# Optimization experiments

Measured on AMD Instinct MI355X. Metric: run time of the kernel, lower is better.

Reference implementation:

```python
import jax, jax.numpy as jnp
import numpy as np

N_FFT = 8192  # config.n (next power of two of 2*seq_len)


def setup_inputs() -> dict:
    key = jax.random.key(0)
    k1, k2, k3, k4 = jax.random.split(key, 4)
    x = jax.random.normal(k1, (2, 4096, 128), dtype=jnp.float32)
    spectral_filters = jax.random.normal(k2, (4096, 16), dtype=jnp.float32)
    # nn.Parameter tensors (zeros in torch init; randomized for a meaningful test)
    M_phi_plus = jax.random.normal(k3, (16, 128, 128), dtype=jnp.float32) * 0.02
    M_phi_minus = jax.random.normal(k4, (16, 128, 128), dtype=jnp.float32) * 0.02
    return {
        "x": x,
        "spectral_filters": spectral_filters,
        "M_phi_plus": M_phi_plus,
        "M_phi_minus": M_phi_minus,
    }


def reference(x, spectral_filters, M_phi_plus, M_phi_minus):
    # STU forward, use_tensordot=False, use_hankel_L=False.
    B, L, D = x.shape
    K = spectral_filters.shape[1]
    n = N_FFT

    # sgn[l] = (-1)^l : the "negative featurization" sign flip
    sgn = jnp.where(jnp.arange(L) % 2 == 0, 1.0, -1.0).astype(x.dtype)  # (L,)

    # FFT of the K spectral filters: (F, K), F = n//2 + 1
    Vf = jnp.fft.rfft(spectral_filters, n=n, axis=0)

    # FFTs of u and sign-flipped u (convolution is linear, so we avoid the
    # torch expand to (B, L, K, D) before the FFT): (B, F, D)
    Uf_plus = jnp.fft.rfft(x, n=n, axis=1)
    Uf_minus = jnp.fft.rfft(x * sgn[None, :, None], n=n, axis=1)

    # Pointwise multiply in frequency, broadcast over K and D: (B, F, K, D)
    U_plus = jnp.fft.irfft(Vf[None, :, :, None] * Uf_plus[:, :, None, :], n=n, axis=1)[:, :L]
    U_minus = jnp.fft.irfft(Vf[None, :, :, None] * Uf_minus[:, :, None, :], n=n, axis=1)[:, :L]
    U_minus = U_minus * sgn[None, :, None, None]  # undo sign on outputs

    # Contract (B, L, K, D) with (K, D, D_out)  ==  reshape(B,L,K*D) @ (K*D, D_out)
    spectral_plus = jnp.einsum("blkd,kde->ble", U_plus, M_phi_plus)
    spectral_minus = jnp.einsum("blkd,kde->ble", U_minus, M_phi_minus)
    return spectral_plus + spectral_minus
```

## Files before the change

### kernel.cpp

```cpp
#include <hip/hip_runtime.h>
#include <stdint.h>

#define N2   8192
#define N    4096
#define LOGN 12
#define F_TOT 4097
#define FP    4112
#define D    128
#define K    16
#define B    2
#define PI_F 3.14159265358979323846f

typedef _Float16 f16x8 __attribute__((ext_vector_type(8)));
typedef float    f32x4 __attribute__((ext_vector_type(4)));

__device__ __forceinline__ void gload_lds16(const void* g, void* l) {
  __builtin_amdgcn_global_load_lds((const __attribute__((address_space(1))) uint32_t*)g,
                                   (__attribute__((address_space(3))) uint32_t*)l, 16, 0, 0);
}

__device__ __forceinline__ int swz(int w) { return w ^ ((w >> 6) & 31); }

__device__ __forceinline__ _Float16 hpick(uint32_t w, int hi) {
  union { unsigned short u; _Float16 h; } c;
  c.u = (unsigned short)(hi ? (w >> 16) : (w & 0xffffu));
  return c.h;
}

__device__ __forceinline__ uint32_t packh2(float a, float b) {
  union { uint32_t u; unsigned short s[2]; } p;
  union { unsigned short u; _Float16 h; } ca, cb;
  ca.h = (_Float16)a; cb.h = (_Float16)b;
  p.s[0] = ca.u; p.s[1] = cb.u;
  return p.u;
}

__device__ __forceinline__ void fft_lds(float* re, float* im, const float2* tw,
                                        int tid, int nthr, float sign) {
  for (int s = 0; s < LOGN; ++s) {
    int len = 1 << s;
    for (int t = tid; t < (N >> 1); t += nthr) {
      int j = t & (len - 1);
      int base = ((t >> s) << (s + 1)) + j;
      int i0 = swz(base), i1 = swz(base + len);
      float2 w = tw[len + j];
      float wr = w.x, wi = sign * w.y;
      float ar = re[i0], ai = im[i0];
      float br = re[i1], bi = im[i1];
      float tr = wr * br - wi * bi;
      float ti = wr * bi + wi * br;
      re[i0] = ar + tr;  im[i0] = ai + ti;
      re[i1] = ar - tr;  im[i1] = ai - ti;
    }
    __syncthreads();
  }
}

__device__ __forceinline__ void fill_tw(float2* tw, int tid, int nthr) {
  for (int i = tid; i < N; i += nthr) {
    if (i >= 1) {
      int s = 31 - __clz(i);
      int j = i - (1 << s);
      float ang = PI_F * (float)j / (float)(1 << s);
      float wi_, wr_; __sincosf(ang, &wi_, &wr_);
      tw[i] = make_float2(wr_, wi_);
    }
  }
}

__global__ __launch_bounds__(256) void transpose_x(const float* __restrict__ x,
                                                   float* __restrict__ xT) {
  __shared__ float t[32][33];
  const int b = blockIdx.z;
  const int l0 = blockIdx.x * 32, d0 = blockIdx.y * 32;
  const int c = threadIdx.x & 31, r0 = threadIdx.x >> 5;
#pragma unroll
  for (int i = 0; i < 4; ++i) {
    int r = r0 + i * 8;
    t[r][c] = x[((size_t)b * N + l0 + r) * D + d0 + c];
  }
  __syncthreads();
#pragma unroll
  for (int i = 0; i < 4; ++i) {
    int r = r0 + i * 8;
    xT[((size_t)b * D + d0 + r) * N + l0 + c] = t[c][r];
  }
}

__global__ __launch_bounds__(512) void fwd_fft(const float* __restrict__ xT,
                                               const float* __restrict__ filt,
                                               const float* __restrict__ Mp,
                                               const float* __restrict__ Mm,
                                               uint32_t* __restrict__ Ufh,
                                               float2* __restrict__ Vf,
                                               _Float16* __restrict__ Mt) {
  __shared__ float re[N];
  __shared__ float im[N];
  __shared__ float2 tw[N];
  const int tid = threadIdx.x;
  const int sig = blockIdx.x;

  if (sig >= B * D + K) {
    const int pid = sig - (B * D + K);
    const int k = pid & 15, h = pid >> 4;
    const float* src = (h ? Mm : Mp) + (size_t)k * D * D;
    for (int d0 = 0; d0 < D; d0 += 16) {
      for (int i = tid; i < 16 * D; i += 512) re[i] = src[(size_t)d0 * D + i];
      __syncthreads();
      if (tid < 256) {
        const int e = tid >> 1, c0 = (tid & 1) * 8;
        f16x8 w;
#pragma unroll
        for (int j = 0; j < 8; ++j) w[j] = (_Float16)re[(c0 + j) * D + e];
        const int eq = e >> 5, el = e & 31;
        const size_t kd8 = (size_t)(d0 + c0) >> 3;
        *(f16x8*)(Mt + (((((size_t)h * 4 + eq) * K + k) * 16 + kd8) * 32 + el) * 8) = w;
      }
      __syncthreads();
    }
    return;
  }

  fill_tw(tw, tid, 512);

  const float* in; int istride;
  int b = 0, d = 0, k = 0;
  const bool isx = sig < B * D;
  if (isx) { b = sig >> 7; d = sig & (D - 1); in = xT + ((size_t)b * D + d) * N; istride = 1; }
  else     { k = sig - B * D; in = filt + k; istride = K; }

  for (int m = tid; m < N; m += 512) {
    float vr = 0.f, vi = 0.f;
    if (m < (N >> 1)) {
      if (istride == 1) { float2 z = ((const float2*)in)[m]; vr = z.x; vi = z.y; }
      else { vr = in[(size_t)(2 * m) * istride]; vi = in[(size_t)(2 * m + 1) * istride]; }
    }
    int dst = swz(__brev(m) >> (32 - LOGN));
    re[dst] = vr; im[dst] = vi;
  }
  __syncthreads();
  fft_lds(re, im, tw, tid, 512, -1.0f);

  for (int f = tid; f <= (N >> 1); f += 512) {
    int f2 = f & (N - 1), fn = (N - f) & (N - 1);
    float zr = re[swz(f2)], zi = im[swz(f2)];
    float nr = re[swz(fn)], ni = im[swz(fn)];
    float Er = 0.5f * (zr + nr), Ei = 0.5f * (zi - ni);
    float Or = 0.5f * (zi + ni), Oi = -0.5f * (zr - nr);
    float ang = -PI_F * (float)f / (float)N;
    float wi_, wr_; __sincosf(ang, &wi_, &wr_);
    float X0r = Er + wr_ * Or - wi_ * Oi;
    float X0i = Ei + wr_ * Oi + wi_ * Or;
    float X1r = Er - wr_ * Or + wi_ * Oi;
    float X1i = -Ei + wr_ * Oi + wi_ * Or;
    if (isx) {
      uint32_t* o = Ufh + ((size_t)b * F_TOT) * D + d;
      o[(size_t)f * D]       = packh2(X0r, X0i);
      o[(size_t)(N - f) * D] = packh2(X1r, X1i);
    } else {
      Vf[(size_t)f * K + k]       = make_float2(X0r, X0i);
      Vf[(size_t)(N - f) * K + k] = make_float2(X1r, X1i);
    }
  }
}

__global__ __launch_bounds__(256, 3) void middle_mfma(const uint32_t* __restrict__ Ufh,
                                                      const float2* __restrict__ Vf,
                                                      const _Float16* __restrict__ Mt,
                                                      float2* __restrict__ Gt) {
  __shared__ __align__(16) char smem[24576];
  float2*   Vl   = (float2*)smem;
  char*     bbuf = smem + 8192;

  const int tid = threadIdx.x;
  const int l = tid & 63, w = tid >> 6;
  const int l15 = l & 15, g = l >> 4;
  const int fg = w >> 1, eg = w & 1;
  const int eq = blockIdx.y, ks = blockIdx.z;
  const int fx = blockIdx.x * 32;
  const int fo = l15 >> 2, bb = (l15 >> 1) & 1, ri = l15 & 1;

  auto STAGE = [&](int buf, int st) {
    const int kg = ks * 8 + (st >> 1), pm = st & 1;
    const _Float16* tile = Mt + (((size_t)pm * 4 + eq) * K + kg) * 4096;
#pragma unroll
    for (int i = 0; i < 2; ++i) {
      const int off = w * 1024 + i * 512;
      gload_lds16((const void*)(tile + off + l * 8),
                  (void*)(bbuf + (size_t)buf * 8192 + (size_t)off * 2));
    }
  };
  STAGE(0, 0);

  {
    const int fl = tid >> 3, kq = tid & 7;
    int fe = fx + fl; if (fe > N) fe = N;
    *(float4*)&Vl[((size_t)0 * 32 + fl) * 16 + kq * 2] =
        *(const float4*)&Vf[(size_t)fe * K + kq * 2];
    *(float4*)&Vl[((size_t)1 * 32 + fl) * 16 + kq * 2] =
        *(const float4*)&Vf[(size_t)(N - fe) * K + kq * 2];
  }

  f16x8 A[4][4];
#pragma unroll
  for (int s = 0; s < 4; ++s) {
    int f = fx + fg * 16 + s * 4 + fo; if (f > N) f = N;
    const uint4* ur = (const uint4*)(Ufh + ((size_t)bb * F_TOT + f) * D);
#pragma unroll
    for (int ds = 0; ds < 4; ++ds) {
      uint4 w0 = ur[ds * 8 + g * 2];
      uint4 w1 = ur[ds * 8 + g * 2 + 1];
      f16x8 a;
      a[0] = hpick(w0.x, ri); a[1] = hpick(w0.y, ri);
      a[2] = hpick(w0.z, ri); a[3] = hpick(w0.w, ri);
      a[4] = hpick(w1.x, ri); a[5] = hpick(w1.y, ri);
      a[6] = hpick(w1.z, ri); a[7] = hpick(w1.w, ri);
      A[s][ds] = a;
    }
  }

  f32x4 acc[4];
#pragma unroll
  for (int s = 0; s < 4; ++s) acc[s] = (f32x4)0.f;

  asm volatile("s_waitcnt vmcnt(0)" ::: "memory");
  __syncthreads();

  int buf = 0;
  for (int st = 0; st < 16; ++st) {
    if (st < 15) STAGE(buf ^ 1, st + 1);
    const int kg = ks * 8 + (st >> 1), pm = st & 1;
    const _Float16* bc = (const _Float16*)(bbuf + (size_t)buf * 8192);

    float2 vv[4];
#pragma unroll
    for (int s = 0; s < 4; ++s)
      vv[s] = Vl[((size_t)pm * 32 + fg * 16 + s * 4 + g) * 16 + kg];

    f32x4 P[4];
#pragma unroll
    for (int ds = 0; ds < 4; ++ds) {
      f16x8 bf = *(const f16x8*)(bc + (size_t)((ds * 4 + g) * 32 + eg * 16 + l15) * 8);
#pragma unroll
      for (int s = 0; s < 4; ++s) {
        f32x4 cin = (ds == 0) ? (f32x4)0.f : P[s];
        P[s] = __builtin_amdgcn_mfma_f32_16x16x32_f16(A[s][ds], bf, cin, 0, 0, 0);
      }
    }
#pragma unroll
    for (int s = 0; s < 4; ++s) {
      const float vr = vv[s].x, vy = vv[s].y;
      if (pm == 0) {
        acc[s][0] += vr * P[s][0] - vy * P[s][1];
        acc[s][1] += vy * P[s][0] + vr * P[s][1];
        acc[s][2] += vr * P[s][2] - vy * P[s][3];
        acc[s][3] += vy * P[s][2] + vr * P[s][3];
      } else {
        acc[s][0] += vr * P[s][0] + vy * P[s][1];
        acc[s][1] += vr * P[s][1] - vy * P[s][0];
        acc[s][2] += vr * P[s][2] + vy * P[s][3];
        acc[s][3] += vr * P[s][3] - vy * P[s][2];
      }
    }
    asm volatile("s_waitcnt vmcnt(0)" ::: "memory");
    __syncthreads();
    buf ^= 1;
  }

  float2* tr = (float2*)smem;
#pragma unroll
  for (int s = 0; s < 4; ++s) {
    const int fl = fg * 16 + s * 4 + g;
    const int el = eg * 16 + l15;
    tr[(size_t)el * 33 + fl]        = make_float2(acc[s][0], acc[s][1]);
    tr[(size_t)(32 + el) * 33 + fl] = make_float2(acc[s][2], acc[s][3]);
  }
  __syncthreads();
  const size_t slab = (size_t)ks * B * D * FP;
#pragma unroll
  for (int p = 0; p < 4; ++p) {
    const int row = p * 16 + (tid >> 4);
    const int bo = row >> 5, e_gl = eq * 32 + (row & 31);
    const int c = (tid & 15) * 2;
    const int fgl = fx + c;
    if (fgl < F_TOT) {
      float2 v0 = tr[(size_t)row * 33 + c], v1 = tr[(size_t)row * 33 + c + 1];
      *(float4*)&Gt[slab + ((size_t)bo * D + e_gl) * FP + fgl] =
          make_float4(v0.x, v0.y, v1.x, v1.y);
    }
  }
}

__global__ __launch_bounds__(512) void inv_fft(const float2* __restrict__ Gt,
                                               float* __restrict__ out) {
  __shared__ float re[N];
  __shared__ float im[N];
  __shared__ float2 tw[N];
  const int tid = threadIdx.x;
  const int sig = blockIdx.x;
  const int b = sig >> 7, e = sig & (D - 1);
  const float2* g0 = Gt + ((size_t)b * D + e) * FP;
  const size_t pstr = (size_t)B * D * FP;

  fill_tw(tw, tid, 512);

  for (int kk = tid; kk <= (N >> 1); kk += 512) {
    float2 a0 = g0[kk],     a1 = g0[pstr + kk];
    float2 b0 = g0[N - kk], b1 = g0[pstr + (N - kk)];
    float Xkx = a0.x + a1.x, Xky = a0.y + a1.y;
    float Xnx = b0.x + b1.x, Xny = b0.y + b1.y;
    float Er = 0.5f * (Xkx + Xnx), Ei = 0.5f * (Xky - Xny);
    float Dr = 0.5f * (Xkx - Xnx), Di = 0.5f * (Xky + Xny);
    float ang = PI_F * (float)kk / (float)N;
    float wi_, wr_; __sincosf(ang, &wi_, &wr_);
    float Or = Dr * wr_ - Di * wi_;
    float Oi = Dr * wi_ + Di * wr_;
    int d1 = swz(__brev(kk) >> (32 - LOGN));
    re[d1] = Er - Oi; im[d1] = Ei + Or;
    if (kk != 0 && kk != (N >> 1)) {
      int d2 = swz(__brev(N - kk) >> (32 - LOGN));
      re[d2] = Er + Oi; im[d2] = -Ei + Or;
    }
  }
  __syncthreads();
  fft_lds(re, im, tw, tid, 512, +1.0f);
  const float scale = 1.0f / (float)N;
  float* ob = out + (size_t)b * N * D + e;
  for (int m = tid; m < (N >> 1); m += 512) {
    int i0 = swz(m);
    ob[(size_t)(2 * m) * D]     = re[i0] * scale;
    ob[(size_t)(2 * m + 1) * D] = im[i0] * scale;
  }
}

extern "C" void kernel_launch(void* const* d_in, const int* in_sizes, int n_in,
                              void* d_out, int out_size, void* d_ws, size_t ws_size,
                              hipStream_t stream) {
  const float* x  = (const float*)d_in[0];
  const float* fl = (const float*)d_in[1];
  const float* Mp = (const float*)d_in[2];
  const float* Mm = (const float*)d_in[3];
  float* out = (float*)d_out;

  float*    xT  = (float*)d_ws;
  uint32_t* Ufh = (uint32_t*)(xT + (size_t)B * D * N);
  float2*   Vf  = (float2*)(Ufh + (size_t)B * F_TOT * D);
  float2*   Gt  = Vf + (size_t)F_TOT * K;
  _Float16* Mt  = (_Float16*)(Gt + (size_t)2 * B * D * FP);

  transpose_x<<<dim3(N / 32, D / 32, B), 256, 0, stream>>>(x, xT);
  fwd_fft<<<B * D + K + 32, 512, 0, stream>>>(xT, fl, Mp, Mm, Ufh, Vf, Mt);
  middle_mfma<<<dim3(129, 4, 2), 256, 0, stream>>>(Ufh, Vf, Mt, Gt);
  inv_fft<<<B * D, 512, 0, stream>>>(Gt, out);
}
```

Baseline: 85.70 us.

## Use radix-4 LDS FFT, padded LDS indexing, and transposed output with separate transpose

The in-LDS FFT moves from radix-2 to radix-4 stages, halving the number of passes and __syncthreads barriers. The XOR swizzle is replaced by padding one word per 32 elements to avoid bank conflicts. The inverse FFT now writes contiguous float2 rows into a scratch buffer (reusing xT), and a new transpose kernel produces the (B,L,D) output, replacing the strided scattered stores. This trades one extra kernel launch and a round trip through global memory for coalesced writes and fewer FFT stages.

```diff
diff --git a/kernel.cpp b/kernel.cpp
--- a/kernel.cpp
+++ b/kernel.cpp
@@ -10,6 +10,7 @@
 #define K    16
 #define B    2
 #define PI_F 3.14159265358979323846f
+#define NPAD (N + (N >> 5))
 
 typedef _Float16 f16x8 __attribute__((ext_vector_type(8)));
 typedef float    f32x4 __attribute__((ext_vector_type(4)));
@@ -19,7 +20,7 @@
                                    (__attribute__((address_space(3))) uint32_t*)l, 16, 0, 0);
 }
 
-__device__ __forceinline__ int swz(int w) { return w ^ ((w >> 6) & 31); }
+__device__ __forceinline__ int pad(int w) { return w + (w >> 5); }
 
 __device__ __forceinline__ _Float16 hpick(uint32_t w, int hi) {
   union { unsigned short u; _Float16 h; } c;
@@ -35,36 +36,49 @@
   return p.u;
 }
 
+__device__ __forceinline__ void fill_tw(float2* tw, int tid, int nthr) {
+  for (int i = tid + 1; i < N; i += nthr) {
+    int s = 31 - __clz(i);
+    int j = i - (1 << s);
+    float ang = PI_F * (float)j / (float)(1 << s);
+    float wi_, wr_; __sincosf(ang, &wi_, &wr_);
+    tw[i] = make_float2(wr_, wi_);
+  }
+}
+
 __device__ __forceinline__ void fft_lds(float* re, float* im, const float2* tw,
                                         int tid, int nthr, float sign) {
-  for (int s = 0; s < LOGN; ++s) {
-    int len = 1 << s;
-    for (int t = tid; t < (N >> 1); t += nthr) {
-      int j = t & (len - 1);
-      int base = ((t >> s) << (s + 1)) + j;
-      int i0 = swz(base), i1 = swz(base + len);
-      float2 w = tw[len + j];
-      float wr = w.x, wi = sign * w.y;
-      float ar = re[i0], ai = im[i0];
-      float br = re[i1], bi = im[i1];
-      float tr = wr * br - wi * bi;
-      float ti = wr * bi + wi * br;
-      re[i0] = ar + tr;  im[i0] = ai + ti;
-      re[i1] = ar - tr;  im[i1] = ai - ti;
+  for (int s = 0; s < LOGN; s += 2) {
+    const int len = 1 << s;
+    for (int t = tid; t < (N >> 2); t += nthr) {
+      const int j = t & (len - 1);
+      const int base = ((t >> s) << (s + 2)) + j;
+      const int i0 = pad(base), i1 = pad(base + len);
+      const int i2 = pad(base + 2 * len), i3 = pad(base + 3 * len);
+      float2 w1 = tw[len + j];
+      float2 w2 = tw[2 * len + j];
+      float2 w3 = tw[3 * len + j];
+      const float w1r = w1.x, w1i = sign * w1.y;
+      const float w2r = w2.x, w2i = sign * w2.y;
+      const float w3r = w3.x, w3i = sign * w3.y;
+      float x0r = re[i0], x0i = im[i0];
+      float x1r = re[i1], x1i = im[i1];
+      float x2r = re[i2], x2i = im[i2];
+      float x3r = re[i3], x3i = im[i3];
+      float t1r = w1r * x1r - w1i * x1i, t1i = w1r * x1i + w1i * x1r;
+      float t3r = w1r * x3r - w1i * x3i, t3i = w1r * x3i + w1i * x3r;
+      float b0r = x0r + t1r, b0i = x0i + t1i;
+      float b1r = x0r - t1r, b1i = x0i - t1i;
+      float b2r = x2r + t3r, b2i = x2i + t3i;
+      float b3r = x2r - t3r, b3i = x2i - t3i;
+      float u2r = w2r * b2r - w2i * b2i, u2i = w2r * b2i + w2i * b2r;
+      float u3r = w3r * b3r - w3i * b3i, u3i = w3r * b3i + w3i * b3r;
+      re[i0] = b0r + u2r; im[i0] = b0i + u2i;
+      re[i2] = b0r - u2r; im[i2] = b0i - u2i;
+      re[i1] = b1r + u3r; im[i1] = b1i + u3i;
+      re[i3] = b1r - u3r; im[i3] = b1i - u3i;
     }
     __syncthreads();
-  }
-}
-
-__device__ __forceinline__ void fill_tw(float2* tw, int tid, int nthr) {
-  for (int i = tid; i < N; i += nthr) {
-    if (i >= 1) {
-      int s = 31 - __clz(i);
-      int j = i - (1 << s);
-      float ang = PI_F * (float)j / (float)(1 << s);
-      float wi_, wr_; __sincosf(ang, &wi_, &wr_);
-      tw[i] = make_float2(wr_, wi_);
-    }
   }
 }
 
@@ -84,6 +98,25 @@
   for (int i = 0; i < 4; ++i) {
     int r = r0 + i * 8;
     xT[((size_t)b * D + d0 + r) * N + l0 + c] = t[c][r];
+  }
+}
+
+__global__ __launch_bounds__(256) void transpose_out(const float* __restrict__ outT,
+                                                     float* __restrict__ out) {
+  __shared__ float t[32][33];
+  const int b = blockIdx.z;
+  const int l0 = blockIdx.x * 32, d0 = blockIdx.y * 32;
+  const int c = threadIdx.x & 31, r0 = threadIdx.x >> 5;
+#pragma unroll
+  for (int i = 0; i < 4; ++i) {
+    int r = r0 + i * 8;
+    t[r][c] = outT[((size_t)b * D + d0 + r) * N + l0 + c];
+  }
+  __syncthreads();
+#pragma unroll
+  for (int i = 0; i < 4; ++i) {
+    int r = r0 + i * 8;
+    out[((size_t)b * N + l0 + r) * D + d0 + c] = t[c][r];
   }
 }
 
@@ -94,8 +127,8 @@
                                                uint32_t* __restrict__ Ufh,
                                                float2* __restrict__ Vf,
                                                _Float16* __restrict__ Mt) {
-  __shared__ float re[N];
-  __shared__ float im[N];
+  __shared__ float re[NPAD];
+  __shared__ float im[NPAD];
   __shared__ float2 tw[N];
   const int tid = threadIdx.x;
   const int sig = blockIdx.x;
@@ -135,7 +168,7 @@
       if (istride == 1) { float2 z = ((const float2*)in)[m]; vr = z.x; vi = z.y; }
       else { vr = in[(size_t)(2 * m) * istride]; vi = in[(size_t)(2 * m + 1) * istride]; }
     }
-    int dst = swz(__brev(m) >> (32 - LOGN));
+    int dst = pad(__brev(m) >> (32 - LOGN));
     re[dst] = vr; im[dst] = vi;
   }
   __syncthreads();
@@ -143,8 +176,8 @@
 
   for (int f = tid; f <= (N >> 1); f += 512) {
     int f2 = f & (N - 1), fn = (N - f) & (N - 1);
-    float zr = re[swz(f2)], zi = im[swz(f2)];
-    float nr = re[swz(fn)], ni = im[swz(fn)];
+    float zr = re[pad(f2)], zi = im[pad(f2)];
+    float nr = re[pad(fn)], ni = im[pad(fn)];
     float Er = 0.5f * (zr + nr), Ei = 0.5f * (zi - ni);
     float Or = 0.5f * (zi + ni), Oi = -0.5f * (zr - nr);
     float ang = -PI_F * (float)f / (float)N;
@@ -292,9 +325,9 @@
 }
 
 __global__ __launch_bounds__(512) void inv_fft(const float2* __restrict__ Gt,
-                                               float* __restrict__ out) {
-  __shared__ float re[N];
-  __shared__ float im[N];
+                                               float* __restrict__ outT) {
+  __shared__ float re[NPAD];
+  __shared__ float im[NPAD];
   __shared__ float2 tw[N];
   const int tid = threadIdx.x;
   const int sig = blockIdx.x;
@@ -315,21 +348,20 @@
     float wi_, wr_; __sincosf(ang, &wi_, &wr_);
     float Or = Dr * wr_ - Di * wi_;
     float Oi = Dr * wi_ + Di * wr_;
-    int d1 = swz(__brev(kk) >> (32 - LOGN));
+    int d1 = pad(__brev(kk) >> (32 - LOGN));
     re[d1] = Er - Oi; im[d1] = Ei + Or;
     if (kk != 0 && kk != (N >> 1)) {
-      int d2 = swz(__brev(N - kk) >> (32 - LOGN));
+      int d2 = pad(__brev(N - kk) >> (32 - LOGN));
       re[d2] = Er + Oi; im[d2] = -Ei + Or;
     }
   }
   __syncthreads();
   fft_lds(re, im, tw, tid, 512, +1.0f);
   const float scale = 1.0f / (float)N;
-  float* ob = out + (size_t)b * N * D + e;
+  float2* ob = (float2*)(outT + ((size_t)b * D + e) * N);
   for (int m = tid; m < (N >> 1); m += 512) {
-    int i0 = swz(m);
-    ob[(size_t)(2 * m) * D]     = re[i0] * scale;
-    ob[(size_t)(2 * m + 1) * D] = im[i0] * scale;
+    int i0 = pad(m);
+    ob[m] = make_float2(re[i0] * scale, im[i0] * scale);
   }
 }
 
@@ -351,5 +383,6 @@
   transpose_x<<<dim3(N / 32, D / 32, B), 256, 0, stream>>>(x, xT);
   fwd_fft<<<B * D + K + 32, 512, 0, stream>>>(xT, fl, Mp, Mm, Ufh, Vf, Mt);
   middle_mfma<<<dim3(129, 4, 2), 256, 0, stream>>>(Ufh, Vf, Mt, Gt);
-  inv_fft<<<B * D, 512, 0, stream>>>(Gt, out);
-}
+  inv_fft<<<B * D, 512, 0, stream>>>(Gt, xT);
+  transpose_out<<<dim3(N / 32, D / 32, B), 256, 0, stream>>>(xT, out);
+}
```

Result: faster. 76.80 us (-10.4%).
